# Kernel tuning notes

Hardware: AMD Instinct MI355X
Metric: run time of the kernel (lower is better)

Reference implementation:

```python
import jax, jax.numpy as jnp
import numpy as np

B, LQ, D_MODEL, H, L_CACHE, WINDOW = 4, 512, 2048, 16, 4096, 4096
D_HEAD = D_MODEL // H
EPS = 1e-8


def setup_inputs() -> dict:
    key = jax.random.key(0)
    ks = jax.random.split(key, 9)
    x_chunk = jax.random.normal(ks[0], (B, LQ, D_MODEL), dtype=jnp.float32)
    # int8-range cache values stored as int32 in [-127, 128)
    k_q = jax.random.randint(ks[1], (B, H, L_CACHE, D_HEAD), 0, 255, dtype=jnp.int32) - 127
    v_q = jax.random.randint(ks[2], (B, H, L_CACHE, D_HEAD), 0, 255, dtype=jnp.int32) - 127
    # per-position scales, typical magnitude amax/127
    k_s = jax.random.uniform(ks[3], (B, H, L_CACHE, 1), dtype=jnp.float32, minval=0.005, maxval=0.03)
    v_s = jax.random.uniform(ks[4], (B, H, L_CACHE, 1), dtype=jnp.float32, minval=0.005, maxval=0.03)
    s = 1.0 / np.sqrt(D_MODEL)
    W_q = jax.random.normal(ks[5], (D_MODEL, D_MODEL), dtype=jnp.float32) * s
    W_k = jax.random.normal(ks[6], (D_MODEL, D_MODEL), dtype=jnp.float32) * s
    W_v = jax.random.normal(ks[7], (D_MODEL, D_MODEL), dtype=jnp.float32) * s
    W_o = jax.random.normal(ks[8], (D_MODEL, D_MODEL), dtype=jnp.float32) * s
    return {"x_chunk": x_chunk, "k_q": k_q, "v_q": v_q, "k_s": k_s, "v_s": v_s,
            "W_q": W_q, "W_k": W_k, "W_v": W_v, "W_o": W_o, "window_size": WINDOW}


def _split_heads(x):  # (B, L, d_model) -> (B, H, L, d_head)
    Bb, L, _ = x.shape
    return x.reshape(Bb, L, H, D_HEAD).transpose(0, 2, 1, 3)


def _merge_heads(x):  # (B, H, L, d_head) -> (B, L, d_model)
    Bb, Hh, L, dh = x.shape
    return x.transpose(0, 2, 1, 3).reshape(Bb, L, Hh * dh)


def quantize_int8_lastdim(x):
    amax = jnp.max(jnp.abs(x), axis=-1, keepdims=True)
    scale = jnp.maximum(amax / 127.0, EPS)
    q = jnp.clip(jnp.round(x / scale), -127, 127).astype(jnp.int8)
    return q, scale.astype(jnp.float16)


def reference(x_chunk, k_q, v_q, k_s, v_s, W_q, W_k, W_v, W_o, window_size):
    Lq = x_chunk.shape[1]
    scale = 1.0 / np.sqrt(D_HEAD)
    q = _split_heads(x_chunk @ W_q.T)
    k_new = _split_heads(x_chunk @ W_k.T)
    v_new = _split_heads(x_chunk @ W_v.T)
    # dequantize int8 KV cache: q * scale (per position)
    k_cache = k_q.astype(jnp.float32) * k_s.astype(jnp.float32)
    v_cache = v_q.astype(jnp.float32) * v_s.astype(jnp.float32)
    k_total = jnp.concatenate([k_cache, k_new], axis=2)  # (B,H,Lk,dh)
    v_total = jnp.concatenate([v_cache, v_new], axis=2)
    Lk_total = k_total.shape[2]
    L_cache = k_cache.shape[2]
    # chunked causal mask with cache offset: key j visible to query i iff j <= L_cache + i
    i = jnp.arange(Lq)[:, None]
    j = jnp.arange(Lk_total)[None, :]
    mask = j > (L_cache + i)  # (Lq, Lk)
    attn = jnp.einsum('bhqd,bhkd->bhqk', q, k_total) * scale
    attn = jnp.where(mask[None, None], jnp.finfo(attn.dtype).min, attn)
    attn = jax.nn.softmax(attn, axis=-1)
    y = jnp.einsum('bhqk,bhkd->bhqd', attn, v_total)
    y = _merge_heads(y) @ W_o.T  # (B, Lq, d_model)
    # sliding-window truncation of cache, then re-quantize
    if Lk_total > window_size:
        k_total = k_total[:, :, -window_size:, :]
        v_total = v_total[:, :, -window_size:, :]
    k_tq, k_scale = quantize_int8_lastdim(k_total)
    v_tq, v_scale = quantize_int8_lastdim(v_total)
    return y, k_tq, v_tq, k_scale, v_scale
```

## Files before the change

### kernel.cpp

```cpp
#include <hip/hip_runtime.h>
#include <hip/hip_fp16.h>

typedef float   f32x4   __attribute__((ext_vector_type(4)));
typedef float   f32x2   __attribute__((ext_vector_type(2)));
typedef float   f32x16  __attribute__((ext_vector_type(16)));
typedef short   short8v __attribute__((ext_vector_type(8)));
typedef unsigned short ushort8v __attribute__((ext_vector_type(8)));
typedef unsigned int   u32x4v __attribute__((ext_vector_type(4)));
typedef unsigned int   u32x2v __attribute__((ext_vector_type(2)));
typedef int     int2v   __attribute__((ext_vector_type(2)));
typedef int     int4v   __attribute__((ext_vector_type(4)));
typedef unsigned int   u32;
typedef unsigned short u16;

#define DEVI static __device__ __forceinline__

DEVI u16 f2bf(float f) {
    u32 u = __builtin_bit_cast(u32, f);
    u += 0x7FFFu + ((u >> 16) & 1u);
    return (u16)(u >> 16);
}
DEVI float bf2f(u16 h) { return __builtin_bit_cast(float, (u32)h << 16); }

DEVI void gl_lds16(const u16* g, u16* l) {
    __builtin_amdgcn_global_load_lds(
        (const __attribute__((address_space(1))) u32*)(const void*)g,
        (__attribute__((address_space(3))) u32*)(void*)l, 16, 0, 0);
}

__global__ __launch_bounds__(256) void convert_kernel(
    const float* __restrict__ src, u16* __restrict__ dst, float scale, int n8) {
    int idx = blockIdx.x * 256 + threadIdx.x;
    if (idx >= n8) return;
    const float* p = src + (size_t)idx * 8;
    f32x4 a = *(const f32x4*)p, b = *(const f32x4*)(p + 4);
    ushort8v o;
    o[0]=f2bf(a[0]*scale); o[1]=f2bf(a[1]*scale); o[2]=f2bf(a[2]*scale); o[3]=f2bf(a[3]*scale);
    o[4]=f2bf(b[0]*scale); o[5]=f2bf(b[1]*scale); o[6]=f2bf(b[2]*scale); o[7]=f2bf(b[3]*scale);
    *(ushort8v*)(dst + (size_t)idx * 8) = o;
}

__global__ __launch_bounds__(256) void convert4_kernel(
    const float* __restrict__ x, const float* __restrict__ Wq,
    const float* __restrict__ Wk, const float* __restrict__ Wv,
    u16* __restrict__ xb, u16* __restrict__ wb3, float rscale) {
    const int seg = blockIdx.x >> 11;
    const int idx = (blockIdx.x & 2047) * 256 + threadIdx.x;
    const float* src; u16* dst; float scale = 1.0f;
    if (seg == 0)      { src = x;  dst = xb; }
    else if (seg == 1) { src = Wq; dst = wb3; scale = rscale; }
    else if (seg == 2) { src = Wk; dst = wb3 + 4194304; }
    else               { src = Wv; dst = wb3 + 8388608; }
    const float* p = src + (size_t)idx * 8;
    f32x4 a = *(const f32x4*)p, b = *(const f32x4*)(p + 4);
    ushort8v o;
    o[0]=f2bf(a[0]*scale); o[1]=f2bf(a[1]*scale); o[2]=f2bf(a[2]*scale); o[3]=f2bf(a[3]*scale);
    o[4]=f2bf(b[0]*scale); o[5]=f2bf(b[1]*scale); o[6]=f2bf(b[2]*scale); o[7]=f2bf(b[3]*scale);
    *(ushort8v*)(dst + (size_t)idx * 8) = o;
}

__global__ __launch_bounds__(256) void prep_cache_kernel(
    const int* __restrict__ kq, const int* __restrict__ vq,
    const float* __restrict__ ks, const float* __restrict__ vs,
    u16* __restrict__ kcb, u16* __restrict__ vt,
    float* __restrict__ oktq, float* __restrict__ ovtq,
    float* __restrict__ oksc, float* __restrict__ ovsc) {
    __shared__ u16 Vs[64][132];
    __shared__ float skL[64], svL[64];
    const int tid = threadIdx.x;
    const int bh = blockIdx.x >> 6, kt = blockIdx.x & 63;
    const int key0 = kt << 6;
    const size_t rowbase = (size_t)bh * 4096 + key0;
    if (tid < 64) { skL[tid] = ks[rowbase + tid]; svL[tid] = vs[rowbase + tid]; }
    __syncthreads();
    const int lane = tid & 63, w = tid >> 6;
    const int q31 = lane & 31, rh = lane >> 5;
    u32x2v* kcw = (u32x2v*)kcb;
    #pragma unroll 4
    for (int s = 0; s < 8; ++s) {
        const int key = s * 8 + w * 2 + rh;
        const size_t row = rowbase + key;
        const float sk = skL[key], sv = svL[key];
        int4v kv = *(const int4v*)(kq + row * 128 + q31 * 4);
        int4v vv = *(const int4v*)(vq + row * 128 + q31 * 4);
        f32x4 kx, vx;
        #pragma unroll
        for (int e = 0; e < 4; ++e) { kx[e] = (float)kv[e] * sk; vx[e] = (float)vv[e] * sv; }
        u32x2v kp, vp;
        kp[0] = (u32)f2bf(kx[0]) | ((u32)f2bf(kx[1]) << 16);
        kp[1] = (u32)f2bf(kx[2]) | ((u32)f2bf(kx[3]) << 16);
        vp[0] = (u32)f2bf(vx[0]) | ((u32)f2bf(vx[1]) << 16);
        vp[1] = (u32)f2bf(vx[2]) | ((u32)f2bf(vx[3]) << 16);
        kcw[(size_t)(bh * 4608 + key0 + key) * 32 + q31] = kp;
        *(u32x2v*)&Vs[key][q31 * 4] = vp;
        float kam = fmaxf(fmaxf(fabsf(kx[0]), fabsf(kx[1])), fmaxf(fabsf(kx[2]), fabsf(kx[3])));
        float vam = fmaxf(fmaxf(fabsf(vx[0]), fabsf(vx[1])), fmaxf(fabsf(vx[2]), fabsf(vx[3])));
        #pragma unroll
        for (int off = 1; off < 32; off <<= 1) {
            kam = fmaxf(kam, __shfl_xor(kam, off, 64));
            vam = fmaxf(vam, __shfl_xor(vam, off, 64));
        }
        const int r = key0 + key;
        if (r >= 512) {
            const size_t orow = (size_t)bh * 4096 + (size_t)(r - 512);
            float kscale = fmaxf(kam / 127.0f, 1e-8f);
            float vscale = fmaxf(vam / 127.0f, 1e-8f);
            float kinv = 1.0f / kscale, vinv = 1.0f / vscale;
            f32x4 ko, vo;
            #pragma unroll
            for (int e = 0; e < 4; ++e) {
                ko[e] = fminf(fmaxf(rintf(kx[e] * kinv), -127.f), 127.f);
                vo[e] = fminf(fmaxf(rintf(vx[e] * vinv), -127.f), 127.f);
            }
            *(f32x4*)(oktq + orow * 128 + q31 * 4) = ko;
            *(f32x4*)(ovtq + orow * 128 + q31 * 4) = vo;
            if (q31 == 0) {
                oksc[orow] = __half2float(__float2half(kscale));
                ovsc[orow] = __half2float(__float2half(vscale));
            }
        }
    }
    __syncthreads();
    const int d = tid >> 1, half = tid & 1;
    u16* obase = vt + ((size_t)bh * 128 + d) * 4608 + key0 + half * 32;
    #pragma unroll
    for (int c = 0; c < 4; ++c) {
        ushort8v tv;
        #pragma unroll
        for (int e = 0; e < 8; ++e) tv[e] = Vs[half * 32 + c * 8 + e][d];
        *(ushort8v*)(obase + c * 8) = tv;
    }
}

__global__ __launch_bounds__(256) void gemm_qkv_kernel(
    const u16* __restrict__ A, const u16* __restrict__ Bw,
    u16* __restrict__ qbf, u16* __restrict__ kcb, u16* __restrict__ vnb) {
    __shared__ u16 As[2][128 * 64];
    __shared__ u16 Bs[2][64 * 64];
    const int tid = threadIdx.x, lane = tid & 63, w = tid >> 6;
    const int sid = (blockIdx.x & 7) * 192 + (blockIdx.x >> 3);
    const int bm = sid & 15, bn = sid >> 4;
    const int m0 = bm * 128, n0 = bn * 64;
    const int wm = (w >> 1) * 64, wn = (w & 1) * 32;
    const int r16 = lane & 15, kb = lane >> 4;

    f32x4 acc[4][2] = {};

    auto stage = [&](int bi, int k0) {
        #pragma unroll
        for (int i = 0; i < 4; ++i) {
            int s = i * 256 + tid;
            int row = s >> 3, l = (s & 7) ^ (row & 7);
            gl_lds16(A + (size_t)(m0 + row) * 2048 + k0 + l * 8,
                     &As[bi][(i * 256 + (tid & ~63)) * 8]);
        }
        #pragma unroll
        for (int i = 0; i < 2; ++i) {
            int s = i * 256 + tid;
            int row = s >> 3, l = (s & 7) ^ (row & 7);
            gl_lds16(Bw + (size_t)(n0 + row) * 2048 + k0 + l * 8,
                     &Bs[bi][(i * 256 + (tid & ~63)) * 8]);
        }
    };

    stage(0, 0);
    __syncthreads();
    int cur = 0;
    for (int t = 0; t < 32; ++t) {
        if (t < 31) stage(cur ^ 1, (t + 1) * 64);
        short8v af[4][2], bf[2][2];
        #pragma unroll
        for (int mf = 0; mf < 4; ++mf) {
            int row = wm + mf * 16 + r16;
            #pragma unroll
            for (int ksv = 0; ksv < 2; ++ksv) {
                int blk = (ksv * 4 + kb) ^ (row & 7);
                af[mf][ksv] = __builtin_bit_cast(short8v,
                    *(const ushort8v*)&As[cur][row * 64 + blk * 8]);
            }
        }
        #pragma unroll
        for (int nf = 0; nf < 2; ++nf) {
            int row = wn + nf * 16 + r16;
            #pragma unroll
            for (int ksv = 0; ksv < 2; ++ksv) {
                int blk = (ksv * 4 + kb) ^ (row & 7);
                bf[nf][ksv] = __builtin_bit_cast(short8v,
                    *(const ushort8v*)&Bs[cur][row * 64 + blk * 8]);
            }
        }
        #pragma unroll
        for (int mf = 0; mf < 4; ++mf)
            #pragma unroll
            for (int nf = 0; nf < 2; ++nf)
                #pragma unroll
                for (int ksv = 0; ksv < 2; ++ksv)
                    acc[mf][nf] = __builtin_amdgcn_mfma_f32_16x16x32_bf16(
                        af[mf][ksv], bf[nf][ksv], acc[mf][nf], 0, 0, 0);
        __syncthreads();
        cur ^= 1;
    }

    #pragma unroll
    for (int mf = 0; mf < 4; ++mf)
        #pragma unroll
        for (int nf = 0; nf < 2; ++nf)
            #pragma unroll
            for (int v = 0; v < 4; ++v) {
                int mg = m0 + wm + mf * 16 + kb * 4 + v;
                int ng = n0 + wn + nf * 16 + r16;
                int nb = ng >> 11, ngl = ng & 2047;
                u16 val = f2bf(acc[mf][nf][v]);
                if (nb == 1) {
                    size_t bh = (size_t)(mg >> 9) * 16 + (ngl >> 7);
                    kcb[(bh * 4608 + 4096 + (mg & 511)) * 128 + (ngl & 127)] = val;
                } else {
                    u16* dst = (nb == 0) ? qbf : vnb;
                    dst[(((size_t)(mg >> 9) * 16 + (ngl >> 7)) * 512 +
                         (mg & 511)) * 128 + (ngl & 127)] = val;
                }
            }
}

__global__ __launch_bounds__(256) void gemm_wo_kernel(
    const u16* __restrict__ A, const u16* __restrict__ Bw,
    float* __restrict__ Cout) {
    __shared__ u16 As[2][128 * 64];
    __shared__ u16 Bs[2][64 * 64];
    const int tid = threadIdx.x, lane = tid & 63, w = tid >> 6;
    const int sid = (blockIdx.x & 7) * 64 + (blockIdx.x >> 3);
    const int bm = sid & 15, bn = sid >> 4;
    const int m0 = bm * 128, n0 = bn * 64;
    const int wm = (w >> 1) * 64, wn = (w & 1) * 32;
    const int r16 = lane & 15, kb = lane >> 4;

    f32x4 acc[4][2] = {};

    auto stage = [&](int bi, int k0) {
        #pragma unroll
        for (int i = 0; i < 4; ++i) {
            int s = i * 256 + tid;
            int row = s >> 3, l = (s & 7) ^ (row & 7);
            gl_lds16(A + (size_t)(m0 + row) * 2048 + k0 + l * 8,
                     &As[bi][(i * 256 + (tid & ~63)) * 8]);
        }
        #pragma unroll
        for (int i = 0; i < 2; ++i) {
            int s = i * 256 + tid;
            int row = s >> 3, l = (s & 7) ^ (row & 7);
            gl_lds16(Bw + (size_t)(n0 + row) * 2048 + k0 + l * 8,
                     &Bs[bi][(i * 256 + (tid & ~63)) * 8]);
        }
    };

    stage(0, 0);
    __syncthreads();
    int cur = 0;
    for (int t = 0; t < 32; ++t) {
        if (t < 31) stage(cur ^ 1, (t + 1) * 64);
        short8v af[4][2], bf[2][2];
        #pragma unroll
        for (int mf = 0; mf < 4; ++mf) {
            int row = wm + mf * 16 + r16;
            #pragma unroll
            for (int ksv = 0; ksv < 2; ++ksv) {
                int blk = (ksv * 4 + kb) ^ (row & 7);
                af[mf][ksv] = __builtin_bit_cast(short8v,
                    *(const ushort8v*)&As[cur][row * 64 + blk * 8]);
            }
        }
        #pragma unroll
        for (int nf = 0; nf < 2; ++nf) {
            int row = wn + nf * 16 + r16;
            #pragma unroll
            for (int ksv = 0; ksv < 2; ++ksv) {
                int blk = (ksv * 4 + kb) ^ (row & 7);
                bf[nf][ksv] = __builtin_bit_cast(short8v,
                    *(const ushort8v*)&Bs[cur][row * 64 + blk * 8]);
            }
        }
        #pragma unroll
        for (int mf = 0; mf < 4; ++mf)
            #pragma unroll
            for (int nf = 0; nf < 2; ++nf)
                #pragma unroll
                for (int ksv = 0; ksv < 2; ++ksv)
                    acc[mf][nf] = __builtin_amdgcn_mfma_f32_16x16x32_bf16(
                        af[mf][ksv], bf[nf][ksv], acc[mf][nf], 0, 0, 0);
        __syncthreads();
        cur ^= 1;
    }

    #pragma unroll
    for (int mf = 0; mf < 4; ++mf)
        #pragma unroll
        for (int nf = 0; nf < 2; ++nf)
            #pragma unroll
            for (int v = 0; v < 4; ++v) {
                int mg = m0 + wm + mf * 16 + kb * 4 + v;
                int ng = n0 + wn + nf * 16 + r16;
                Cout[(size_t)mg * 2048 + ng] = acc[mf][nf][v];
            }
}

__global__ __launch_bounds__(256) void quant_new_kernel(
    const u16* __restrict__ kcb, const u16* __restrict__ vnb,
    u16* __restrict__ vt,
    float* __restrict__ oktq, float* __restrict__ ovtq,
    float* __restrict__ oksc, float* __restrict__ ovsc) {
    __shared__ u16 Vs[64][132];
    const int tid = threadIdx.x;
    const int bh = blockIdx.x >> 3, kt = blockIdx.x & 7;
    const int i0 = kt << 6;
    const int lane = tid & 63, w = tid >> 6;
    const int q31 = lane & 31, rh = lane >> 5;
    #pragma unroll 4
    for (int s = 0; s < 8; ++s) {
        const int key = s * 8 + w * 2 + rh;
        const int i = i0 + key;
        u32x2v ku = *(const u32x2v*)(kcb + ((size_t)bh * 4608 + 4096 + i) * 128 + q31 * 4);
        u32x2v vu = *(const u32x2v*)(vnb + ((size_t)bh * 512 + i) * 128 + q31 * 4);
        f32x4 kx, vx;
        kx[0] = bf2f((u16)ku[0]); kx[1] = bf2f((u16)(ku[0] >> 16));
        kx[2] = bf2f((u16)ku[1]); kx[3] = bf2f((u16)(ku[1] >> 16));
        vx[0] = bf2f((u16)vu[0]); vx[1] = bf2f((u16)(vu[0] >> 16));
        vx[2] = bf2f((u16)vu[1]); vx[3] = bf2f((u16)(vu[1] >> 16));
        *(u32x2v*)&Vs[key][q31 * 4] = vu;
        float kam = fmaxf(fmaxf(fabsf(kx[0]), fabsf(kx[1])), fmaxf(fabsf(kx[2]), fabsf(kx[3])));
        float vam = fmaxf(fmaxf(fabsf(vx[0]), fabsf(vx[1])), fmaxf(fabsf(vx[2]), fabsf(vx[3])));
        #pragma unroll
        for (int off = 1; off < 32; off <<= 1) {
            kam = fmaxf(kam, __shfl_xor(kam, off, 64));
            vam = fmaxf(vam, __shfl_xor(vam, off, 64));
        }
        float kscale = fmaxf(kam / 127.0f, 1e-8f);
        float vscale = fmaxf(vam / 127.0f, 1e-8f);
        float kinv = 1.0f / kscale, vinv = 1.0f / vscale;
        const size_t orow = (size_t)bh * 4096 + 3584 + i;
        f32x4 ko, vo;
        #pragma unroll
        for (int e = 0; e < 4; ++e) {
            ko[e] = fminf(fmaxf(rintf(kx[e] * kinv), -127.f), 127.f);
            vo[e] = fminf(fmaxf(rintf(vx[e] * vinv), -127.f), 127.f);
        }
        *(f32x4*)(oktq + orow * 128 + q31 * 4) = ko;
        *(f32x4*)(ovtq + orow * 128 + q31 * 4) = vo;
        if (q31 == 0) {
            oksc[orow] = __half2float(__float2half(kscale));
            ovsc[orow] = __half2float(__float2half(vscale));
        }
    }
    __syncthreads();
    const int d = tid >> 1, half = tid & 1;
    u16* obase = vt + ((size_t)bh * 128 + d) * 4608 + 4096 + i0 + half * 32;
    #pragma unroll
    for (int c = 0; c < 4; ++c) {
        ushort8v tv;
        #pragma unroll
        for (int e = 0; e < 8; ++e) tv[e] = Vs[half * 32 + c * 8 + e][d];
        *(ushort8v*)(obase + c * 8) = tv;
    }
}

__global__ __launch_bounds__(256, 2) void attn_kernel(
    const u16* __restrict__ qb, const u16* __restrict__ kcb,
    const u16* __restrict__ vt, u16* __restrict__ Op0, u16* __restrict__ Op1,
    float* __restrict__ mlp) {
    __shared__ u16 Ks[2][64 * 128];
    __shared__ u16 Vl[2][128 * 64];

    const int tid = threadIdx.x, lane = tid & 63, w = tid >> 6;
    const int p = blockIdx.x;
    const int xcd = p & 7, i = p >> 3;
    const int qt2 = i & 3, sp = (i >> 2) & 1;
    const int bh = ((i >> 3) << 3) | xcd;
    const int q31 = lane & 31, hi = lane >> 5;
    const int qrow = qt2 * 128 + w * 32 + q31;

    const u16* qp = qb + ((size_t)bh * 512 + qrow) * 128 + hi * 8;
    short8v qf[8];
    #pragma unroll
    for (int s = 0; s < 8; ++s)
        qf[s] = __builtin_bit_cast(short8v, *(const ushort8v*)(qp + s * 16));

    f32x16 O[4] = {};
    float m_i = -3.0e38f, l_i = 0.f;

    const size_t kbase = (size_t)bh * 4608 * 128;
    const size_t vbase = (size_t)bh * 128 * 4608;
    const int ktA = sp ? 32 : 0;
    const int ktB = sp ? (66 + 2 * qt2) : 32;

    auto STAGE = [&](int bi, int kt) {
        #pragma unroll
        for (int ii = 0; ii < 4; ++ii) {
            int s = ii * 256 + tid;
            int row = s >> 4, l = (s & 15) ^ (row & 7);
            gl_lds16(kcb + kbase + (size_t)(kt * 64 + row) * 128 + l * 8,
                     &Ks[bi][(ii * 256 + (tid & ~63)) * 8]);
        }
        #pragma unroll
        for (int ii = 0; ii < 4; ++ii) {
            int s = ii * 256 + tid;
            int row = s >> 3, l = (s & 7) ^ (row & 7);
            gl_lds16(vt + vbase + (size_t)row * 4608 + kt * 64 + l * 8,
                     &Vl[bi][(ii * 256 + (tid & ~63)) * 8]);
        }
    };

    STAGE(0, ktA);
    __syncthreads();
    int cur = 0;
    for (int kt = ktA; kt < ktB; ++kt) {
        if (kt + 1 < ktB) STAGE(cur ^ 1, kt + 1);

        f32x16 S[2] = {};
        __builtin_amdgcn_s_setprio(1);
        #pragma unroll
        for (int s = 0; s < 8; ++s) {
            #pragma unroll
            for (int t = 0; t < 2; ++t) {
                int krow = t * 32 + q31;
                int blk = (2 * s + hi) ^ (krow & 7);
                short8v kf = __builtin_bit_cast(short8v,
                    *(const ushort8v*)&Ks[cur][krow * 128 + blk * 8]);
                S[t] = __builtin_amdgcn_mfma_f32_32x32x16_bf16(kf, qf[s], S[t], 0, 0, 0);
            }
        }
        __builtin_amdgcn_s_setprio(0);

        if (kt >= 64) {
            const int kb0 = (kt - 64) * 64 + 4 * hi;
            #pragma unroll
            for (int r = 0; r < 16; ++r) {
                int koff = kb0 + (r & 3) + 8 * (r >> 2);
                if (koff > qrow)      S[0][r] = -3.0e38f;
                if (koff + 32 > qrow) S[1][r] = -3.0e38f;
            }
        }

        float mx = fmaxf(S[0][0], S[1][0]);
        #pragma unroll
        for (int r = 1; r < 16; ++r) mx = fmaxf(mx, fmaxf(S[0][r], S[1][r]));
        mx = fmaxf(mx, __shfl_xor(mx, 32, 64));

        if (__ballot(mx > m_i + 8.f)) {
            float mnew = fmaxf(m_i, mx);
            float alpha = __expf(m_i - mnew);
            m_i = mnew;
            l_i *= alpha;
            #pragma unroll
            for (int r = 0; r < 16; ++r) {
                float ar = __shfl(alpha, (r & 3) + 8 * (r >> 2) + 4 * hi, 64);
                O[0][r] *= ar; O[1][r] *= ar; O[2][r] *= ar; O[3][r] *= ar;
            }
        }
        #pragma unroll
        for (int r = 0; r < 16; ++r) {
            S[0][r] = __expf(S[0][r] - m_i); l_i += S[0][r];
            S[1][r] = __expf(S[1][r] - m_i); l_i += S[1][r];
        }

        __builtin_amdgcn_s_setprio(1);
        #pragma unroll
        for (int j = 0; j < 4; ++j) {
            const int t = j >> 1, r0 = 8 * (j & 1);
            u32 a0, a1, b0, b1;
            asm("v_cvt_pk_bf16_f32 %0, %1, %2" : "=v"(a0) : "v"(S[t][r0+0]), "v"(S[t][r0+1]));
            asm("v_cvt_pk_bf16_f32 %0, %1, %2" : "=v"(a1) : "v"(S[t][r0+2]), "v"(S[t][r0+3]));
            asm("v_cvt_pk_bf16_f32 %0, %1, %2" : "=v"(b0) : "v"(S[t][r0+4]), "v"(S[t][r0+5]));
            asm("v_cvt_pk_bf16_f32 %0, %1, %2" : "=v"(b1) : "v"(S[t][r0+6]), "v"(S[t][r0+7]));
            asm("v_permlane32_swap_b32 %0, %1" : "+v"(a0), "+v"(b0));
            asm("v_permlane32_swap_b32 %0, %1" : "+v"(a1), "+v"(b1));
            u32x4v pw = {a0, a1, b0, b1};
            short8v pf = __builtin_bit_cast(short8v, pw);
            #pragma unroll
            for (int od = 0; od < 4; ++od) {
                int vrow = od * 32 + q31;
                int blk = (2 * j + hi) ^ (vrow & 7);
                short8v vf = __builtin_bit_cast(short8v,
                    *(const ushort8v*)&Vl[cur][vrow * 64 + blk * 8]);
                O[od] = __builtin_amdgcn_mfma_f32_32x32x16_bf16(pf, vf, O[od], 0, 0, 0);
            }
        }
        __builtin_amdgcn_s_setprio(0);

        __syncthreads();
        cur ^= 1;
    }

    float lt = l_i + __shfl_xor(l_i, 32, 64);
    u16* Op = sp ? Op1 : Op0;
    const size_t pbase = ((size_t)bh * 4 + qt2) * 16384;
    #pragma unroll
    for (int r = 0; r < 16; ++r) {
        int qoff = (r & 3) + 8 * (r >> 2) + 4 * hi;
        size_t rowb = pbase + (size_t)(w * 32 + qoff) * 128 + q31;
        Op[rowb +  0] = f2bf(O[0][r]);
        Op[rowb + 32] = f2bf(O[1][r]);
        Op[rowb + 64] = f2bf(O[2][r]);
        Op[rowb + 96] = f2bf(O[3][r]);
    }
    if (hi == 0) {
        int qg = ((sp * 256 + bh * 4 + qt2) * 128 + w * 32 + q31);
        mlp[qg * 2 + 0] = m_i;
        mlp[qg * 2 + 1] = lt;
    }
}

__global__ __launch_bounds__(256) void combine_kernel(
    const u16* __restrict__ Op0, const u16* __restrict__ Op1,
    const float* __restrict__ mlp, u16* __restrict__ yb) {
    const int p = blockIdx.x;
    const int bh = p >> 2, qt2 = p & 3;
    const int b = bh >> 4, h = bh & 15;
    const int q = threadIdx.x >> 1, dh = threadIdx.x & 1;
    const int base = (bh * 4 + qt2) * 128 + q;
    float m0 = mlp[base * 2], l0 = mlp[base * 2 + 1];
    float m1 = mlp[(256 * 128 + base) * 2], l1 = mlp[(256 * 128 + base) * 2 + 1];
    float M = fmaxf(m0, m1);
    float a0 = __expf(m0 - M), a1 = __expf(m1 - M);
    float invL = 1.0f / (l0 * a0 + l1 * a1);
    a0 *= invL; a1 *= invL;
    const size_t pb = ((size_t)bh * 4 + qt2) * 16384 + (size_t)q * 128 + dh * 64;
    u16* dst = yb + ((size_t)(b * 512 + qt2 * 128 + q)) * 2048 + h * 128 + dh * 64;
    #pragma unroll
    for (int j = 0; j < 8; ++j) {
        ushort8v o0 = *(const ushort8v*)(Op0 + pb + j * 8);
        ushort8v o1 = *(const ushort8v*)(Op1 + pb + j * 8);
        ushort8v o;
        #pragma unroll
        for (int e = 0; e < 8; ++e)
            o[e] = f2bf(bf2f(o0[e]) * a0 + bf2f(o1[e]) * a1);
        *(ushort8v*)(dst + j * 8) = o;
    }
}

extern "C" void kernel_launch(void* const* d_in, const int* in_sizes, int n_in,
                              void* d_out, int out_size, void* d_ws, size_t ws_size,
                              hipStream_t stream) {
    (void)in_sizes; (void)n_in; (void)out_size; (void)ws_size;
    const float* x   = (const float*)d_in[0];
    const int*   kq  = (const int*)d_in[1];
    const int*   vq  = (const int*)d_in[2];
    const float* ks  = (const float*)d_in[3];
    const float* vs  = (const float*)d_in[4];
    const float* Wq  = (const float*)d_in[5];
    const float* Wk  = (const float*)d_in[6];
    const float* Wv  = (const float*)d_in[7];
    const float* Wo  = (const float*)d_in[8];

    float* out  = (float*)d_out;
    float* y_o  = out;
    float* oktq = out + 4194304;
    float* ovtq = out + 37748736;
    float* oksc = out + 71303168;
    float* ovsc = out + 71565312;
    float* mlp  = out;

    char* wsb = (char*)d_ws;
    u16* kcb = (u16*)(wsb);
    u16* vtb = (u16*)(wsb + 75497472);
    u16* xb  = (u16*)(wsb + 150994944);
    u16* qbf = (u16*)(wsb + 159383552);
    u16* vnb = (u16*)(wsb + 167772160);
    u16* ybf = (u16*)(wsb + 176160768);
    u16* wb3 = (u16*)(wsb + 184549376);

    const float rscale = 0.08838834764831845f;
    const int n8 = 2048 * 2048 / 8;

    prep_cache_kernel<<<4096, 256, 0, stream>>>(kq, vq, ks, vs, kcb, vtb,
                                                oktq, ovtq, oksc, ovsc);
    convert4_kernel<<<8192, 256, 0, stream>>>(x, Wq, Wk, Wv, xb, wb3, rscale);
    gemm_qkv_kernel<<<1536, 256, 0, stream>>>(xb, wb3, qbf, kcb, vnb);
    quant_new_kernel<<<512, 256, 0, stream>>>(kcb, vnb, vtb,
                                              oktq, ovtq, oksc, ovsc);
    attn_kernel<<<512, 256, 0, stream>>>(qbf, kcb, vtb, xb, vnb, mlp);
    combine_kernel<<<256, 256, 0, stream>>>(xb, vnb, mlp, ybf);
    convert_kernel<<<2048, 256, 0, stream>>>(Wo, wb3, 1.0f, n8);
    gemm_wo_kernel<<<512, 256, 0, stream>>>(ybf, wb3, y_o);
}
```

Before: 403.7 us.

## Fuse cache prep and QKV GEMM into one interleaved launch

The memory-bound KV cache dequant/requant prep and the compute-bound QKV GEMM are merged into a single kernel whose blocks are interleaved 8 prep to 3 GEMM. Both share one 48KB shared buffer, so bandwidth-heavy and MFMA-heavy work can run on the CUs at the same time. Prep blocks now also carry the larger shared allocation and a 3-blocks-per-CU launch bound, which may lower their occupancy. Each block writes to separate regions of kcb (cache part versus new-key part), so the two kinds of work do not conflict.

```diff
diff --git a/kernel.cpp b/kernel.cpp
--- a/kernel.cpp
+++ b/kernel.cpp
@@ -59,16 +59,17 @@
     *(ushort8v*)(dst + (size_t)idx * 8) = o;
 }
 
-__global__ __launch_bounds__(256) void prep_cache_kernel(
+DEVI void prep_body(int pid, char* LB,
     const int* __restrict__ kq, const int* __restrict__ vq,
     const float* __restrict__ ks, const float* __restrict__ vs,
     u16* __restrict__ kcb, u16* __restrict__ vt,
     float* __restrict__ oktq, float* __restrict__ ovtq,
     float* __restrict__ oksc, float* __restrict__ ovsc) {
-    __shared__ u16 Vs[64][132];
-    __shared__ float skL[64], svL[64];
+    u16 (*Vs)[132] = (u16(*)[132])LB;
+    float* skL = (float*)(LB + 16896);
+    float* svL = (float*)(LB + 17152);
     const int tid = threadIdx.x;
-    const int bh = blockIdx.x >> 6, kt = blockIdx.x & 63;
+    const int bh = pid >> 6, kt = pid & 63;
     const int key0 = kt << 6;
     const size_t rowbase = (size_t)bh * 4096 + key0;
     if (tid < 64) { skL[tid] = ks[rowbase + tid]; svL[tid] = vs[rowbase + tid]; }
@@ -132,13 +133,13 @@
     }
 }
 
-__global__ __launch_bounds__(256) void gemm_qkv_kernel(
+DEVI void qkv_body(int qid, char* LB,
     const u16* __restrict__ A, const u16* __restrict__ Bw,
     u16* __restrict__ qbf, u16* __restrict__ kcb, u16* __restrict__ vnb) {
-    __shared__ u16 As[2][128 * 64];
-    __shared__ u16 Bs[2][64 * 64];
+    u16* As = (u16*)LB;
+    u16* Bs = (u16*)(LB + 32768);
     const int tid = threadIdx.x, lane = tid & 63, w = tid >> 6;
-    const int sid = (blockIdx.x & 7) * 192 + (blockIdx.x >> 3);
+    const int sid = (qid & 7) * 192 + (qid >> 3);
     const int bm = sid & 15, bn = sid >> 4;
     const int m0 = bm * 128, n0 = bn * 64;
     const int wm = (w >> 1) * 64, wn = (w & 1) * 32;
@@ -152,14 +153,14 @@
             int s = i * 256 + tid;
             int row = s >> 3, l = (s & 7) ^ (row & 7);
             gl_lds16(A + (size_t)(m0 + row) * 2048 + k0 + l * 8,
-                     &As[bi][(i * 256 + (tid & ~63)) * 8]);
+                     &As[bi * 8192 + (i * 256 + (tid & ~63)) * 8]);
         }
         #pragma unroll
         for (int i = 0; i < 2; ++i) {
             int s = i * 256 + tid;
             int row = s >> 3, l = (s & 7) ^ (row & 7);
             gl_lds16(Bw + (size_t)(n0 + row) * 2048 + k0 + l * 8,
-                     &Bs[bi][(i * 256 + (tid & ~63)) * 8]);
+                     &Bs[bi * 4096 + (i * 256 + (tid & ~63)) * 8]);
         }
     };
 
@@ -176,7 +177,7 @@
             for (int ksv = 0; ksv < 2; ++ksv) {
                 int blk = (ksv * 4 + kb) ^ (row & 7);
                 af[mf][ksv] = __builtin_bit_cast(short8v,
-                    *(const ushort8v*)&As[cur][row * 64 + blk * 8]);
+                    *(const ushort8v*)&As[cur * 8192 + row * 64 + blk * 8]);
             }
         }
         #pragma unroll
@@ -186,7 +187,7 @@
             for (int ksv = 0; ksv < 2; ++ksv) {
                 int blk = (ksv * 4 + kb) ^ (row & 7);
                 bf[nf][ksv] = __builtin_bit_cast(short8v,
-                    *(const ushort8v*)&Bs[cur][row * 64 + blk * 8]);
+                    *(const ushort8v*)&Bs[cur * 4096 + row * 64 + blk * 8]);
             }
         }
         #pragma unroll
@@ -220,6 +221,24 @@
                          (mg & 511)) * 128 + (ngl & 127)] = val;
                 }
             }
+}
+
+__global__ __launch_bounds__(256, 3) void fused_prep_qkv_kernel(
+    const int* __restrict__ kq, const int* __restrict__ vq,
+    const float* __restrict__ ks, const float* __restrict__ vs,
+    u16* __restrict__ kcb, u16* __restrict__ vt,
+    float* __restrict__ oktq, float* __restrict__ ovtq,
+    float* __restrict__ oksc, float* __restrict__ ovsc,
+    const u16* __restrict__ xb, const u16* __restrict__ wb3,
+    u16* __restrict__ qbf, u16* __restrict__ vnb) {
+    __shared__ __align__(16) char LB[49152];
+    const int grp = blockIdx.x / 11, rem = blockIdx.x % 11;
+    if (rem < 8) {
+        prep_body(grp * 8 + rem, LB, kq, vq, ks, vs, kcb, vt,
+                  oktq, ovtq, oksc, ovsc);
+    } else {
+        qkv_body(grp * 3 + (rem - 8), LB, xb, wb3, qbf, kcb, vnb);
+    }
 }
 
 __global__ __launch_bounds__(256) void gemm_wo_kernel(
@@ -570,10 +589,10 @@
     const float rscale = 0.08838834764831845f;
     const int n8 = 2048 * 2048 / 8;
 
-    prep_cache_kernel<<<4096, 256, 0, stream>>>(kq, vq, ks, vs, kcb, vtb,
-                                                oktq, ovtq, oksc, ovsc);
     convert4_kernel<<<8192, 256, 0, stream>>>(x, Wq, Wk, Wv, xb, wb3, rscale);
-    gemm_qkv_kernel<<<1536, 256, 0, stream>>>(xb, wb3, qbf, kcb, vnb);
+    fused_prep_qkv_kernel<<<5632, 256, 0, stream>>>(
+        kq, vq, ks, vs, kcb, vtb, oktq, ovtq, oksc, ovsc,
+        xb, wb3, qbf, vnb);
     quant_new_kernel<<<512, 256, 0, stream>>>(kcb, vnb, vtb,
                                               oktq, ovtq, oksc, ovsc);
     attn_kernel<<<512, 256, 0, stream>>>(qbf, kcb, vtb, xb, vnb, mlp);
```

New measurement: 419.4 us. 1.04x slower.
